# Kernel tuning notes

Hardware: AMD Instinct MI355X
Metric: run time of the kernel (lower is better)

## Reference

```python
import jax, jax.numpy as jnp
import numpy as np
import math

B, N, T, F_IN, F_OUT = 8, 512, 12, 32, 64


def setup_inputs() -> dict:
    key = jax.random.key(0)
    k1, k2, k3, k4, k5 = jax.random.split(key, 5)
    x = jax.random.normal(k1, (B, N, T, F_IN), dtype=jnp.float32)
    phaseAct_matrix = jax.random.uniform(k2, (B, T, N, N), dtype=jnp.float32)
    adj = jax.random.uniform(k3, (N, N), dtype=jnp.float32)  # sym-normalized adjacency stand-in
    mask = (jax.random.uniform(k4, (N,)) < 0.5).astype(jnp.float32)  # 1 = observed node, 0 = unknown
    theta = jax.random.normal(k5, (F_IN, F_OUT), dtype=jnp.float32) * 0.05
    return {"x": x, "phaseAct_matrix": phaseAct_matrix, "adj": adj, "mask": mask, "theta": theta}


def _spatial_attention(x):
    # x: (B, N, T, F) -> scores (B, T, N, N)
    f = x.shape[-1]
    xt = x.transpose(0, 2, 1, 3)  # (B, T, N, F)
    score = jnp.einsum('btnf,btmf->btnm', xt, xt) / math.sqrt(f)
    return jax.nn.softmax(score, axis=-1)


def reference(x, phaseAct_matrix, adj, mask, theta):
    f = x.shape[-1]
    t_steps = x.shape[2]
    inv_sqrt_f = 1.0 / math.sqrt(f)
    m = mask[None, :, None, None]  # broadcast over (B, N, T-1, F)

    def body(i, x_cur):
        sa = _spatial_attention(x_cur) * inv_sqrt_f          # (B, T, N, N)
        sat_act = (phaseAct_matrix * sa).transpose(0, 1, 3, 2)  # (B, T, N, N) transposed
        xt = x_cur.transpose(0, 2, 1, 3)                     # (B, T, N, F)
        # predict step t from step t-1: (B, T-1, N, F)
        x_pred = jnp.einsum('btnm,btmf->btnf', sat_act[:, 1:], xt[:, :t_steps - 1])
        x_pred = x_pred.transpose(0, 2, 1, 3)                # (B, N, T-1, F)
        # revise_unknown: keep observed nodes, impute unknown nodes at steps 1..T-1
        x_rev = x_cur[:, :, 1:, :] * m + x_pred * (1.0 - m)
        return jnp.concatenate([x_cur[:, :, 0:1, :], x_rev], axis=2)

    x = jax.lax.fori_loop(1, t_steps, body, x)

    sa = _spatial_attention(x) * inv_sqrt_f                  # (B, T, N, N)
    satAct_adj = phaseAct_matrix * adj[None, None] * sa      # (B, T, N, N)
    xt = x.transpose(0, 2, 1, 3)                             # (B, T, N, F)
    agg = jnp.einsum('btmn,btmf->btnf', satAct_adj, xt)      # transpose(adj) @ x
    out = jax.nn.relu(jnp.einsum('btnf,fo->btno', agg, theta))  # (B, T, N, F_out)
    return out.transpose(0, 2, 1, 3)                         # (B, N, T, F_out)
```

## Files before the change

kernel.cpp:

```cpp
#include <hip/hip_runtime.h>


#define B_ 8
#define N_ 512
#define T_ 12
#define F_ 32
#define O_ 64
#define MT 8
#define NW 8

typedef unsigned int uint_t;
typedef unsigned short ushort_t;
typedef _Float16 f16_t;
typedef _Float16 f16x4 __attribute__((ext_vector_type(4)));
typedef _Float16 f16x8 __attribute__((ext_vector_type(8)));
typedef float f32x4 __attribute__((ext_vector_type(4)));

__device__ __forceinline__ void atomAddF(float* p, float v) {
    __hip_atomic_fetch_add(p, v, __ATOMIC_RELAXED, __HIP_MEMORY_SCOPE_AGENT);
}
__device__ __forceinline__ int xidx(int b, int n, int t, int f) {
    return ((b * N_ + n) * T_ + t) * F_ + f;
}
__device__ __forceinline__ f16x8 load_frag8(const float* p) {
    float4 a = *reinterpret_cast<const float4*>(p);
    float4 b = *reinterpret_cast<const float4*>(p + 4);
    f16x8 r;
    r[0] = (f16_t)a.x; r[1] = (f16_t)a.y; r[2] = (f16_t)a.z; r[3] = (f16_t)a.w;
    r[4] = (f16_t)b.x; r[5] = (f16_t)b.y; r[6] = (f16_t)b.z; r[7] = (f16_t)b.w;
    return r;
}
union U2H4 { uint2 u; f16x4 h; };

__global__ __launch_bounds__(256)
void permute_kernel(const float* __restrict__ src, ushort_t* __restrict__ dst)
{
    __shared__ float Lp[16][516];
    const int tid = threadIdx.x;
    const int mc  = blockIdx.x;
    const int s   = blockIdx.y;
    src += (size_t)s * N_ * N_ + (size_t)mc * 16 * N_;
    uint_t* dstu = (uint_t*)dst + (size_t)s * 131072 + (size_t)mc * 4096;

    #pragma unroll
    for (int k = 0; k < 32; ++k) {
        int idx = tid + 256 * k;
        Lp[idx >> 9][idx & 511] = src[idx];
    }
    __syncthreads();
    #pragma unroll
    for (int k = 0; k < 16; ++k) {
        int u    = tid + 256 * k;
        int nt   = u >> 7;
        int r    = u & 127;
        int quad = r >> 5;
        int cl   = (r >> 1) & 15;
        int m0   = quad * 4 + (r & 1) * 2;
        int n    = nt * 16 + cl;
        union { f16_t h[2]; uint_t i; } pk;
        pk.h[0] = (f16_t)Lp[m0][n];
        pk.h[1] = (f16_t)Lp[m0 + 1][n];
        dstu[u] = pk.i;
    }
}

template <int FINAL>
__global__ __launch_bounds__(512)
void gcn_kernel(const float* __restrict__ x0,
                const float* __restrict__ xcur,
                float* __restrict__ dst,
                const ushort_t* __restrict__ phase_h,
                const ushort_t* __restrict__ adj_h,
                const float* __restrict__ mask)
{
    __shared__ float2 st[2][NW][16];

    const int tid  = threadIdx.x;
    const int w    = tid >> 6;
    const int l    = tid & 63;
    const int quad = l >> 4;
    const int col  = l & 15;
    const int mt   = blockIdx.x;
    const int t    = FINAL ? blockIdx.y : blockIdx.y + 1;
    const int b    = blockIdx.z;
    const int nt0  = w * 4;
    const float inv_f = 0.17677669529663687f;

    const float* xs     = (FINAL && t == 0) ? x0 : xcur;
    const float* xp_src = FINAL ? xs : ((t == 1) ? x0 : xcur);
    const int    tp     = FINAL ? t : t - 1;

    f16x8 bf[4];
    #pragma unroll
    for (int i = 0; i < 4; ++i)
        bf[i] = load_frag8(&xs[xidx(b, (nt0 + i) * 16 + col, t, quad * 8)]);

    f32x4 acc[4][2];
    #pragma unroll
    for (int i = 0; i < 4; ++i) {
        acc[i][0] = (f32x4){0.f, 0.f, 0.f, 0.f};
        acc[i][1] = (f32x4){0.f, 0.f, 0.f, 0.f};
    }

    const uint_t* phu = (const uint_t*)phase_h + (size_t)(b * T_ + t) * 131072;
    const uint_t* adu = (const uint_t*)adj_h;

    for (int c = 0; c < 512 / (MT * 16); ++c) {
        const int mb = mt * (N_ / MT) + c * 16;
        const int mc = mb >> 4;

        f16x8 af = load_frag8(&xs[xidx(b, mb + col, t, quad * 8)]);

        U2H4 ph[4], aj[4];
        #pragma unroll
        for (int i = 0; i < 4; ++i) {
            ph[i].u = *(const uint2*)(phu + (size_t)mc * 4096 + (nt0 + i) * 128 + l * 2);
            if (FINAL)
                aj[i].u = *(const uint2*)(adu + (size_t)mc * 4096 + (nt0 + i) * 128 + l * 2);
        }
        f16x4 bp[2];
        #pragma unroll
        for (int ft = 0; ft < 2; ++ft)
            #pragma unroll
            for (int j = 0; j < 4; ++j)
                bp[ft][j] = (f16_t)xp_src[xidx(b, mb + quad * 4 + j, tp, ft * 16 + col)];

        f32x4 s4[4];
        #pragma unroll
        for (int i = 0; i < 4; ++i) {
            s4[i] = __builtin_amdgcn_mfma_f32_16x16x32_f16(
                        af, bf[i], (f32x4){0.f, 0.f, 0.f, 0.f}, 0, 0, 0);
        }
        float mxw[4], sw[4], e[4][4];
        #pragma unroll
        for (int v = 0; v < 4; ++v) {
            #pragma unroll
            for (int i = 0; i < 4; ++i) s4[i][v] *= inv_f;
            mxw[v] = fmaxf(fmaxf(s4[0][v], s4[1][v]), fmaxf(s4[2][v], s4[3][v]));
        }
        #pragma unroll
        for (int d = 1; d < 16; d <<= 1)
            #pragma unroll
            for (int v = 0; v < 4; ++v)
                mxw[v] = fmaxf(mxw[v], __shfl_xor(mxw[v], d, 64));
        #pragma unroll
        for (int v = 0; v < 4; ++v) {
            #pragma unroll
            for (int i = 0; i < 4; ++i) e[i][v] = __expf(s4[i][v] - mxw[v]);
            sw[v] = (e[0][v] + e[1][v]) + (e[2][v] + e[3][v]);
        }
        #pragma unroll
        for (int d = 1; d < 16; d <<= 1)
            #pragma unroll
            for (int v = 0; v < 4; ++v)
                sw[v] += __shfl_xor(sw[v], d, 64);

        const int buf = c & 1;
        if (col < 4) {
            float mv = (col == 0) ? mxw[0] : (col == 1) ? mxw[1] : (col == 2) ? mxw[2] : mxw[3];
            float sv = (col == 0) ? sw[0]  : (col == 1) ? sw[1]  : (col == 2) ? sw[2]  : sw[3];
            st[buf][w][quad * 4 + col] = make_float2(mv, sv);
        }
        __syncthreads();
        {
            const int row = l >> 2, wp = l & 3;
            float2 p0 = st[buf][2 * wp][row];
            float2 p1 = st[buf][2 * wp + 1][row];
            float M = fmaxf(p0.x, p1.x);
            float S = p0.y * __expf(p0.x - M) + p1.y * __expf(p1.x - M);
            #pragma unroll
            for (int d = 1; d < 4; d <<= 1) {
                float Mo = __shfl_xor(M, d, 64), So = __shfl_xor(S, d, 64);
                float Mn = fmaxf(M, Mo);
                S = S * __expf(M - Mn) + So * __expf(Mo - Mn);
                M = Mn;
            }
            #pragma unroll
            for (int v = 0; v < 4; ++v) {
                float Mr = __shfl(M, quad * 16 + v * 4, 64);
                float Sr = __shfl(S, quad * 16 + v * 4, 64);
                mxw[v] = __expf(mxw[v] - Mr) * inv_f / Sr;
            }
        }

        #pragma unroll
        for (int i = 0; i < 4; ++i) {
            f16x4 wf;
            if (FINAL) {
                #pragma unroll
                for (int v = 0; v < 4; ++v)
                    wf[v] = (f16_t)(e[i][v] * mxw[v] * (float)ph[i].h[v] * (float)aj[i].h[v]);
            } else {
                #pragma unroll
                for (int v = 0; v < 4; ++v)
                    wf[v] = (f16_t)(e[i][v] * mxw[v] * (float)ph[i].h[v]);
            }
            #pragma unroll
            for (int ft = 0; ft < 2; ++ft)
                acc[i][ft] = __builtin_amdgcn_mfma_f32_16x16x16f16(wf, bp[ft], acc[i][ft], 0, 0, 0);
        }
    }

    #pragma unroll
    for (int i = 0; i < 4; ++i) {
        #pragma unroll
        for (int v = 0; v < 4; ++v) {
            const int n = (nt0 + i) * 16 + quad * 4 + v;
            if (FINAL) {
                float* d0 = &dst[((b * T_ + t) * N_ + n) * F_ + col];
                atomAddF(d0, acc[i][0][v]);
                atomAddF(d0 + 16, acc[i][1][v]);
            } else if (mask[n] == 0.f) {
                atomAddF(&dst[xidx(b, n, t, col)], acc[i][0][v]);
                atomAddF(&dst[xidx(b, n, t, 16 + col)], acc[i][1][v]);
            }
        }
    }
    if (!FINAL && mt == 0) {
        for (int p = tid; p < N_ * F_; p += 512) {
            int n = p >> 5, f = p & 31;
            if (mask[n] != 0.f) dst[xidx(b, n, t, f)] = xcur[xidx(b, n, t, f)];
        }
    }
}

__global__ __launch_bounds__(256)
void proj_kernel(const float* __restrict__ agg, const float* __restrict__ theta,
                 float* __restrict__ out)
{
    __shared__ float th[F_ * O_];
    int tid = threadIdx.x;
    #pragma unroll
    for (int p = 0; p < 8; ++p) th[tid + 256 * p] = theta[tid + 256 * p];
    __syncthreads();
    int g  = blockIdx.x * 256 + tid;
    int o  = g & 63;
    int r  = g >> 6;
    int tt = r % T_;
    int r2 = r / T_;
    int n  = r2 & 511;
    int b  = r2 >> 9;
    const float* a = &agg[((b * T_ + tt) * N_ + n) * F_];
    float s = 0.f;
    #pragma unroll
    for (int f = 0; f < F_; ++f) s += a[f] * th[f * O_ + o];
    out[g] = fmaxf(s, 0.f);
}

extern "C" void kernel_launch(void* const* d_in, const int* in_sizes, int n_in,
                              void* d_out, int out_size, void* d_ws, size_t ws_size,
                              hipStream_t stream)
{
    const float* x     = (const float*)d_in[0];
    const float* phase = (const float*)d_in[1];
    const float* adj   = (const float*)d_in[2];
    const float* mask  = (const float*)d_in[3];
    const float* theta = (const float*)d_in[4];
    float* out = (float*)d_out;

    const size_t XE = (size_t)B_ * N_ * T_ * F_;
    float*    xA      = (float*)d_ws;
    float*    xB      = xA + XE;
    float*    agg     = xB + XE;
    ushort_t* phase_h = (ushort_t*)(agg + XE);
    ushort_t* adj_h   = phase_h + (size_t)96 * N_ * N_;

    permute_kernel<<<dim3(32, 96), 256, 0, stream>>>(phase, phase_h);
    permute_kernel<<<dim3(32, 1), 256, 0, stream>>>(adj, adj_h);

    const float* cur = x;
    float* bufs[2] = { xA, xB };
    for (int i = 0; i < T_ - 1; ++i) {
        float* nxt = bufs[i & 1];
        hipMemsetAsync(nxt, 0, XE * sizeof(float), stream);
        gcn_kernel<0><<<dim3(MT, T_ - 1, B_), 512, 0, stream>>>(
            x, cur, nxt, phase_h, adj_h, mask);
        cur = nxt;
    }
    hipMemsetAsync(agg, 0, XE * sizeof(float), stream);
    gcn_kernel<1><<<dim3(MT, T_, B_), 512, 0, stream>>>(
        x, cur, agg, phase_h, adj_h, mask);
    proj_kernel<<<(B_ * N_ * T_ * O_) / 256, 256, 0, stream>>>(agg, theta, out);
}
```

Before: 1.101 ms.

## Drop split-K atomics: one block per (b,t) reduces all columns, no memsets

```diff
diff --git a/kernel.cpp b/kernel.cpp
--- a/kernel.cpp
+++ b/kernel.cpp
@@ -6,7 +6,7 @@
 #define T_ 12
 #define F_ 32
 #define O_ 64
-#define MT 8
+#define MT 1
 #define NW 8
 
 typedef unsigned int uint_t;
@@ -16,9 +16,6 @@
 typedef _Float16 f16x8 __attribute__((ext_vector_type(8)));
 typedef float f32x4 __attribute__((ext_vector_type(4)));
 
-__device__ __forceinline__ void atomAddF(float* p, float v) {
-    __hip_atomic_fetch_add(p, v, __ATOMIC_RELAXED, __HIP_MEMORY_SCOPE_AGENT);
-}
 __device__ __forceinline__ int xidx(int b, int n, int t, int f) {
     return ((b * N_ + n) * T_ + t) * F_ + f;
 }
@@ -80,7 +77,6 @@
     const int l    = tid & 63;
     const int quad = l >> 4;
     const int col  = l & 15;
-    const int mt   = blockIdx.x;
     const int t    = FINAL ? blockIdx.y : blockIdx.y + 1;
     const int b    = blockIdx.z;
     const int nt0  = w * 4;
@@ -106,8 +102,8 @@
     const uint_t* adu = (const uint_t*)adj_h;
 
     for (int c = 0; c < 512 / (MT * 16); ++c) {
-        const int mb = mt * (N_ / MT) + c * 16;
-        const int mc = mb >> 4;
+        const int mb = c * 16;
+        const int mc = c;
 
         f16x8 af = load_frag8(&xs[xidx(b, mb + col, t, quad * 8)]);
 
@@ -208,18 +204,16 @@
             const int n = (nt0 + i) * 16 + quad * 4 + v;
             if (FINAL) {
                 float* d0 = &dst[((b * T_ + t) * N_ + n) * F_ + col];
-                atomAddF(d0, acc[i][0][v]);
-                atomAddF(d0 + 16, acc[i][1][v]);
-            } else if (mask[n] == 0.f) {
-                atomAddF(&dst[xidx(b, n, t, col)], acc[i][0][v]);
-                atomAddF(&dst[xidx(b, n, t, 16 + col)], acc[i][1][v]);
-            }
-        }
-    }
-    if (!FINAL && mt == 0) {
-        for (int p = tid; p < N_ * F_; p += 512) {
-            int n = p >> 5, f = p & 31;
-            if (mask[n] != 0.f) dst[xidx(b, n, t, f)] = xcur[xidx(b, n, t, f)];
+                d0[0]  = acc[i][0][v];
+                d0[16] = acc[i][1][v];
+            } else {
+                const int i0 = xidx(b, n, t, col);
+                const float mk  = mask[n];
+                const float xc0 = xcur[i0];
+                const float xc1 = xcur[i0 + 16];
+                dst[i0]      = (mk != 0.f) ? xc0 : acc[i][0][v];
+                dst[i0 + 16] = (mk != 0.f) ? xc1 : acc[i][1][v];
+            }
         }
     }
 }
@@ -272,13 +266,11 @@
     float* bufs[2] = { xA, xB };
     for (int i = 0; i < T_ - 1; ++i) {
         float* nxt = bufs[i & 1];
-        hipMemsetAsync(nxt, 0, XE * sizeof(float), stream);
-        gcn_kernel<0><<<dim3(MT, T_ - 1, B_), 512, 0, stream>>>(
+        gcn_kernel<0><<<dim3(1, T_ - 1, B_), 512, 0, stream>>>(
             x, cur, nxt, phase_h, adj_h, mask);
         cur = nxt;
     }
-    hipMemsetAsync(agg, 0, XE * sizeof(float), stream);
-    gcn_kernel<1><<<dim3(MT, T_, B_), 512, 0, stream>>>(
+    gcn_kernel<1><<<dim3(1, T_, B_), 512, 0, stream>>>(
         x, cur, agg, phase_h, adj_h, mask);
     proj_kernel<<<(B_ * N_ * T_ * O_) / 256, 256, 0, stream>>>(agg, theta, out);
 }
```

After: 1.061 ms. 3.6% less time.
